# Kernel optimization log

Hardware: AMD Instinct MI355X
Metric: run time of the kernel (lower is better)

The kernel has to match this reference:

```python
import jax, jax.numpy as jnp
import numpy as np

F = 256

def setup_inputs() -> dict:
    key = jax.random.key(0)
    ks = jax.random.split(key, 6)
    s = 1.0 / np.sqrt(F)
    x = jax.random.normal(ks[0], (16, 1024, F), dtype=jnp.float32)
    W_alpha = jax.random.uniform(ks[1], (F, F), minval=-s, maxval=s, dtype=jnp.float32)
    W_beta = jax.random.uniform(ks[2], (F, F), minval=-s, maxval=s, dtype=jnp.float32)
    W_unary = jax.random.uniform(ks[3], (F, F), minval=-s, maxval=s, dtype=jnp.float32)
    b_unary = jax.random.uniform(ks[4], (F,), minval=-s, maxval=s, dtype=jnp.float32)
    W_r = jax.random.uniform(ks[5], (F, F), minval=-s, maxval=s, dtype=jnp.float32)
    return {"x": x, "W_alpha": W_alpha, "W_beta": W_beta, "W_unary": W_unary, "b_unary": b_unary, "W_r": W_r}

def reference(x, W_alpha, W_beta, W_unary, b_unary, W_r):
    # x: [B, N, F]; torch Linear computes x @ W^T (+ b)
    B, N, _ = x.shape
    alpha = jnp.einsum('bnf,gf->bng', x, W_alpha)
    beta = jnp.einsum('bnf,gf->bng', x, W_beta)
    unary = jnp.einsum('bnf,gf->bng', x, W_unary) + b_unary
    # scores: alpha_i . beta_j, diagonal excluded (i == j skipped in loop)
    scores = jnp.einsum('bif,bjf->bij', alpha, beta)
    scores = scores * (1.0 - jnp.eye(N, dtype=x.dtype))
    att = jnp.einsum('bij,bjf->bif', scores, unary) / N
    out = jnp.einsum('bif,gf->big', att, W_r) + x
    return out
```

## Files before the change

### kernel.cpp

```cpp
#include <hip/hip_runtime.h>


typedef __bf16 bf16;
typedef float floatx4 __attribute__((ext_vector_type(4)));
typedef bf16 bf16x8 __attribute__((ext_vector_type(8)));
typedef bf16 bf16x4 __attribute__((ext_vector_type(4)));

constexpr int FD = 256;
constexpr int NB = 16;
constexpr int NN = 1024;
constexpr int RR = NB * NN;

__device__ __forceinline__ bf16x8 cvt8(float4 a, float4 b) {
    bf16x8 o = { (bf16)a.x, (bf16)a.y, (bf16)a.z, (bf16)a.w,
                 (bf16)b.x, (bf16)b.y, (bf16)b.z, (bf16)b.w };
    return o;
}

__global__ __launch_bounds__(256)
void prep(const float* __restrict__ Wa, const float* __restrict__ Wb,
          const float* __restrict__ Wu, const float* __restrict__ bu,
          const float* __restrict__ Wr,
          bf16* __restrict__ Wcb, bf16* __restrict__ Wab, float* __restrict__ bc)
{
    const int blk = blockIdx.x, tid = threadIdx.x;
    if (blk < 256) {
        const int j = blk;
        float acc = 0.0f;
        for (int g = 0; g < FD; g += 4) {
            float4 wr = *(const float4*)&Wr[j * FD + g];
            acc += wr.x * Wu[g * FD + tid] + wr.y * Wu[(g + 1) * FD + tid]
                 + wr.z * Wu[(g + 2) * FD + tid] + wr.w * Wu[(g + 3) * FD + tid];
        }
        Wcb[j * FD + tid] = (bf16)acc;
    } else if (blk == 256) {
        float s = 0.0f;
        for (int g = 0; g < FD; g++) s += Wr[tid * FD + g] * bu[g];
        bc[tid] = s;
    } else {
        const int f = blk - 257;
        float acc = 0.0f;
        for (int k = 0; k < FD; k += 4) {
            acc += Wa[k * FD + f] * Wb[k * FD + tid]
                 + Wa[(k + 1) * FD + f] * Wb[(k + 1) * FD + tid]
                 + Wa[(k + 2) * FD + f] * Wb[(k + 2) * FD + tid]
                 + Wa[(k + 3) * FD + f] * Wb[(k + 3) * FD + tid];
        }
        Wab[f * FD + tid] = (bf16)acc;
    }
}

__global__ __launch_bounds__(256)
void proj2(const float* __restrict__ x,
           const bf16* __restrict__ Wab, const bf16* __restrict__ Wc,
           bf16* __restrict__ U2, bf16* __restrict__ abT, bf16* __restrict__ U2T,
           const float* __restrict__ bc, float* __restrict__ dpart)
{
    constexpr int BM = 128, BN = 64, BK = 32, LDK = 36;
    __shared__ bf16 As[BM][LDK];
    __shared__ bf16 Bs[2][BN][LDK];
    __shared__ bf16 Tr[8960];
    const int tid = threadIdx.x;
    const int wave = tid >> 6, lane = tid & 63;
    const int q = lane >> 4, l16 = lane & 15;
    const int bm = blockIdx.y * BM, bn = blockIdx.x * BN;

    const int rowA0 = tid >> 2,          k8A0 = (tid & 3) * 8;
    const int rowA1 = (tid + 256) >> 2,  k8A1 = (tid & 3) * 8;
    const int rowW  = tid >> 2,          k8W  = (tid & 3) * 8;

    bf16x8 pxa0, pxa1; int4 pwq, pwc;
#define PROJ_LOAD(KK) do { \
        const float* s0 = &x[(size_t)(bm + rowA0) * FD + (KK) + k8A0]; \
        pxa0 = cvt8(*(const float4*)s0, *(const float4*)(s0 + 4)); \
        const float* s1 = &x[(size_t)(bm + rowA1) * FD + (KK) + k8A1]; \
        pxa1 = cvt8(*(const float4*)s1, *(const float4*)(s1 + 4)); \
        pwq = *(const int4*)&Wab[(size_t)(bn + rowW) * FD + (KK) + k8W]; \
        pwc = *(const int4*)&Wc[(size_t)(bn + rowW) * FD + (KK) + k8W]; \
    } while (0)

    floatx4 acc[2][2][4] = {};
    PROJ_LOAD(0);

    for (int k0 = 0; k0 < FD; k0 += BK) {
        *(bf16x8*)&As[rowA0][k8A0] = pxa0;
        *(bf16x8*)&As[rowA1][k8A1] = pxa1;
        *(int4*)&Bs[0][rowW][k8W] = pwq;
        *(int4*)&Bs[1][rowW][k8W] = pwc;
        __syncthreads();
        if (k0 + BK < FD) PROJ_LOAD(k0 + BK);
        bf16x8 af[2];
        #pragma unroll
        for (int mi = 0; mi < 2; mi++)
            af[mi] = *(const bf16x8*)&As[wave * 32 + mi * 16 + l16][q * 8];
        #pragma unroll
        for (int w = 0; w < 2; w++) {
            bf16x8 bq[4];
            #pragma unroll
            for (int nj = 0; nj < 4; nj++)
                bq[nj] = *(const bf16x8*)&Bs[w][nj * 16 + l16][q * 8];
            #pragma unroll
            for (int mi = 0; mi < 2; mi++)
                #pragma unroll
                for (int nj = 0; nj < 4; nj++)
                    acc[w][mi][nj] = __builtin_amdgcn_mfma_f32_16x16x32_bf16(af[mi], bq[nj], acc[w][mi][nj], 0, 0, 0);
        }
        __syncthreads();
    }
#undef PROJ_LOAD

    const int b = bm >> 10, n0 = bm & (NN - 1);
    float bcv[4];
    #pragma unroll
    for (int nj = 0; nj < 4; nj++) bcv[nj] = bc[bn + nj * 16 + l16];

    #pragma unroll
    for (int mi = 0; mi < 2; mi++)
        #pragma unroll
        for (int i = 0; i < 4; i++) {
            const int m = bm + wave * 32 + mi * 16 + q * 4 + i;
            float p = 0.0f;
            #pragma unroll
            for (int nj = 0; nj < 4; nj++)
                p += x[(size_t)m * FD + bn + nj * 16 + l16] * acc[0][mi][nj][i];
            #pragma unroll
            for (int off = 1; off < 16; off <<= 1) p += __shfl_xor(p, off);
            if (l16 == 0) dpart[(size_t)blockIdx.x * RR + m] = p;
        }

    __syncthreads();
    #pragma unroll
    for (int mi = 0; mi < 2; mi++)
        #pragma unroll
        for (int i = 0; i < 4; i++) {
            int ml = wave * 32 + mi * 16 + q * 4 + i;
            #pragma unroll
            for (int nj = 0; nj < 4; nj++)
                Tr[ml * 68 + nj * 16 + l16] = (bf16)(acc[1][mi][nj][i] + bcv[nj]);
        }
    __syncthreads();
    #pragma unroll
    for (int it = 0; it < 4; it++) {
        int c = tid + it * 256;
        int row = c >> 3, chunk = c & 7;
        bf16x8 v = *(const bf16x8*)&Tr[row * 68 + chunk * 8];
        *(bf16x8*)&U2[(size_t)(bm + row) * FD + bn + chunk * 8] = v;
    }

    #pragma unroll
    for (int pass = 0; pass < 2; pass++) {
        __syncthreads();
        #pragma unroll
        for (int mi = 0; mi < 2; mi++)
            #pragma unroll
            for (int nj = 0; nj < 4; nj++) {
                bf16x4 v4;
                #pragma unroll
                for (int i = 0; i < 4; i++) {
                    float v = acc[pass][mi][nj][i];
                    if (pass == 1) v += bcv[nj];
                    v4[i] = (bf16)v;
                }
                *(bf16x4*)&Tr[(nj * 16 + l16) * 140 + wave * 32 + mi * 16 + q * 4] = v4;
            }
        __syncthreads();
        bf16* dst = (pass ? U2T : abT) + (size_t)b * FD * NN;
        #pragma unroll
        for (int it = 0; it < 4; it++) {
            int c = tid + it * 256;
            int row = c >> 4, chunk = c & 15;
            bf16x8 v = *(const bf16x8*)&Tr[row * 140 + chunk * 8];
            *(bf16x8*)&dst[(size_t)(bn + row) * NN + n0 + chunk * 8] = v;
        }
    }
}

__global__ __launch_bounds__(256)
void m2_mfma(const bf16* __restrict__ U2T, const bf16* __restrict__ abT, bf16* __restrict__ G)
{
    constexpr int LDK = 72;
    __shared__ bf16 As[64][LDK];
    __shared__ bf16 Bs[64][LDK];
    __shared__ bf16 Tr[64 * 68];
    const int tid = threadIdx.x;
    const int wave = tid >> 6, lane = tid & 63;
    const int q = lane >> 4, l16 = lane & 15;
    const int wj = wave >> 1, wk = wave & 1;
    const int b = blockIdx.z;
    const int bj = blockIdx.y * 64, bk = blockIdx.x * 64;
    const int r0 = tid >> 3,         k80 = (tid & 7) * 8;
    const int r1 = (tid + 256) >> 3, k81 = (tid & 7) * 8;
    const bf16* Arow0 = U2T + (size_t)b * FD * NN + (size_t)(bj + r0) * NN + k80;
    const bf16* Arow1 = U2T + (size_t)b * FD * NN + (size_t)(bj + r1) * NN + k81;
    const bf16* Brow0 = abT + (size_t)b * FD * NN + (size_t)(bk + r0) * NN + k80;
    const bf16* Brow1 = abT + (size_t)b * FD * NN + (size_t)(bk + r1) * NN + k81;

    int4 ra0 = *(const int4*)&Arow0[0];
    int4 ra1 = *(const int4*)&Arow1[0];
    int4 rb0 = *(const int4*)&Brow0[0];
    int4 rb1 = *(const int4*)&Brow1[0];
    floatx4 acc[2][2] = {};
    for (int n0 = 0; n0 < NN; n0 += 64) {
        *(int4*)&As[r0][k80] = ra0;
        *(int4*)&As[r1][k81] = ra1;
        *(int4*)&Bs[r0][k80] = rb0;
        *(int4*)&Bs[r1][k81] = rb1;
        __syncthreads();
        if (n0 + 64 < NN) {
            ra0 = *(const int4*)&Arow0[n0 + 64];
            ra1 = *(const int4*)&Arow1[n0 + 64];
            rb0 = *(const int4*)&Brow0[n0 + 64];
            rb1 = *(const int4*)&Brow1[n0 + 64];
        }
        #pragma unroll
        for (int kk = 0; kk < 2; kk++) {
            bf16x8 af[2], bq[2];
            #pragma unroll
            for (int mi = 0; mi < 2; mi++)
                af[mi] = *(const bf16x8*)&As[wj * 32 + mi * 16 + l16][kk * 32 + q * 8];
            #pragma unroll
            for (int kj = 0; kj < 2; kj++)
                bq[kj] = *(const bf16x8*)&Bs[wk * 32 + kj * 16 + l16][kk * 32 + q * 8];
            #pragma unroll
            for (int mi = 0; mi < 2; mi++)
                #pragma unroll
                for (int kj = 0; kj < 2; kj++)
                    acc[mi][kj] = __builtin_amdgcn_mfma_f32_16x16x32_bf16(af[mi], bq[kj], acc[mi][kj], 0, 0, 0);
        }
        __syncthreads();
    }
    __syncthreads();
    #pragma unroll
    for (int mi = 0; mi < 2; mi++)
        #pragma unroll
        for (int i = 0; i < 4; i++) {
            int jl = wj * 32 + mi * 16 + q * 4 + i;
            #pragma unroll
            for (int kj = 0; kj < 2; kj++)
                Tr[jl * 68 + wk * 32 + kj * 16 + l16] = (bf16)acc[mi][kj][i];
        }
    __syncthreads();
    bf16* Gb = G + (size_t)b * FD * FD;
    #pragma unroll
    for (int it = 0; it < 2; it++) {
        int c = tid + it * 256;
        int r = c >> 3, chunk = c & 7;
        bf16x8 v = *(const bf16x8*)&Tr[r * 68 + chunk * 8];
        *(bf16x8*)&Gb[(size_t)(bj + r) * FD + bk + chunk * 8] = v;
    }
}

__global__ __launch_bounds__(256)
void final_mfma(const float* __restrict__ x, const bf16* __restrict__ G,
                const float* __restrict__ dpart, const bf16* __restrict__ U2,
                float* __restrict__ out)
{
    constexpr int BM = 128, BN = 64, BK = 32, LDK = 36;
    __shared__ bf16 As[BM][LDK];
    __shared__ bf16 Bs[BN][LDK];
    const int tid = threadIdx.x;
    const int wave = tid >> 6, lane = tid & 63;
    const int q = lane >> 4, l16 = lane & 15;
    const int bm = blockIdx.y * BM, bn = blockIdx.x * BN;
    const bf16* Gb = G + (size_t)(bm >> 10) * FD * FD;

    const int rowA0 = tid >> 2,         k8A0 = (tid & 3) * 8;
    const int rowA1 = (tid + 256) >> 2, k8A1 = (tid & 3) * 8;
    const int rowB  = tid >> 2,         k8B  = (tid & 3) * 8;

    bf16x8 ra0, ra1; int4 rb;
#define FIN_LOAD(KK) do { \
        const float* s0 = &x[(size_t)(bm + rowA0) * FD + (KK) + k8A0]; \
        ra0 = cvt8(*(const float4*)s0, *(const float4*)(s0 + 4)); \
        const float* s1 = &x[(size_t)(bm + rowA1) * FD + (KK) + k8A1]; \
        ra1 = cvt8(*(const float4*)s1, *(const float4*)(s1 + 4)); \
        rb = *(const int4*)&Gb[(size_t)(bn + rowB) * FD + (KK) + k8B]; \
    } while (0)

    floatx4 acc[2][4] = {};
    FIN_LOAD(0);
    for (int k0 = 0; k0 < FD; k0 += BK) {
        *(bf16x8*)&As[rowA0][k8A0] = ra0;
        *(bf16x8*)&As[rowA1][k8A1] = ra1;
        *(int4*)&Bs[rowB][k8B] = rb;
        __syncthreads();
        if (k0 + BK < FD) FIN_LOAD(k0 + BK);
        bf16x8 af[2], bq[4];
        #pragma unroll
        for (int mi = 0; mi < 2; mi++)
            af[mi] = *(const bf16x8*)&As[wave * 32 + mi * 16 + l16][q * 8];
        #pragma unroll
        for (int nj = 0; nj < 4; nj++)
            bq[nj] = *(const bf16x8*)&Bs[nj * 16 + l16][q * 8];
        #pragma unroll
        for (int mi = 0; mi < 2; mi++)
            #pragma unroll
            for (int nj = 0; nj < 4; nj++)
                acc[mi][nj] = __builtin_amdgcn_mfma_f32_16x16x32_bf16(af[mi], bq[nj], acc[mi][nj], 0, 0, 0);
        __syncthreads();
    }
#undef FIN_LOAD

    #pragma unroll
    for (int mi = 0; mi < 2; mi++)
        #pragma unroll
        for (int i = 0; i < 4; i++) {
            int m = bm + wave * 32 + mi * 16 + q * 4 + i;
            float d = dpart[m] + dpart[RR + m] + dpart[2 * RR + m] + dpart[3 * RR + m];
            #pragma unroll
            for (int nj = 0; nj < 4; nj++) {
                int n = bn + nj * 16 + l16;
                float v = (acc[mi][nj][i] - d * (float)U2[(size_t)m * FD + n]) * (1.0f / 1024.0f);
                out[(size_t)m * FD + n] = v + x[(size_t)m * FD + n];
            }
        }
}

extern "C" void kernel_launch(void* const* d_in, const int* in_sizes, int n_in,
                              void* d_out, int out_size, void* d_ws, size_t ws_size,
                              hipStream_t stream)
{
    const float* x  = (const float*)d_in[0];
    const float* Wa = (const float*)d_in[1];
    const float* Wb = (const float*)d_in[2];
    const float* Wu = (const float*)d_in[3];
    const float* bu = (const float*)d_in[4];
    const float* Wr = (const float*)d_in[5];
    float* out = (float*)d_out;

    char* w = (char*)d_ws;
    bf16* Wcb   = (bf16*)w;  w += (size_t)FD * FD * 2;
    bf16* Wab   = (bf16*)w;  w += (size_t)FD * FD * 2;
    float* bc   = (float*)w; w += (size_t)FD * 4;
    bf16* U2    = (bf16*)w;  w += (size_t)RR * FD * 2;
    bf16* abT   = (bf16*)w;  w += (size_t)RR * FD * 2;
    bf16* U2T   = (bf16*)w;  w += (size_t)RR * FD * 2;
    bf16* G     = (bf16*)w;  w += (size_t)NB * FD * FD * 2;
    float* dpart= (float*)w; w += (size_t)4 * RR * 4;

    dim3 blk(256);

    prep<<<dim3(513), blk, 0, stream>>>(Wa, Wb, Wu, bu, Wr, Wcb, Wab, bc);

    proj2<<<dim3(FD / 64, RR / 128), blk, 0, stream>>>(x, Wab, Wcb,
                                                       U2, abT, U2T, bc, dpart);

    m2_mfma<<<dim3(FD / 64, FD / 64, NB), blk, 0, stream>>>(U2T, abT, G);

    final_mfma<<<dim3(FD / 64, RR / 128), blk, 0, stream>>>(x, G, dpart, U2, out);
}
```

Measured before the change: 133.0 us.

## Fuse projection, Gram and final kernels into one persistent kernel with grid barriers

Merges the three main kernels into a single 512-block kernel that uses atomic-counter grid barriers between phases, with shared memory overlaid through a union. The m2 stage is retiled to 64x32 output tiles so its work fills all 512 blocks. This removes two kernel launches and their tail gaps. In exchange the grid barrier spins on a global atomic, and the code relies on all 512 blocks being co-resident (launch bounds ask for two per CU), otherwise it can deadlock.

```diff
diff --git a/kernel.cpp b/kernel.cpp
--- a/kernel.cpp
+++ b/kernel.cpp
@@ -17,11 +17,28 @@
     return o;
 }
 
+struct P1s { bf16 As[128][36]; bf16 Bs[2][64][36]; bf16 Tr[8960]; };
+struct P2s { bf16 As[64][72];  bf16 Bs[32][72];    bf16 Tr[64*36]; };
+struct P3s { bf16 As[128][36]; bf16 Bs[64][36]; };
+union SMem { P1s p1; P2s p2; P3s p3; };
+
+__device__ __forceinline__ void grid_barrier(int* cnt, int target) {
+    __syncthreads();
+    if (threadIdx.x == 0) {
+        __threadfence();
+        __hip_atomic_fetch_add(cnt, 1, __ATOMIC_ACQ_REL, __HIP_MEMORY_SCOPE_AGENT);
+        while (__hip_atomic_load(cnt, __ATOMIC_ACQUIRE, __HIP_MEMORY_SCOPE_AGENT) < target)
+            __builtin_amdgcn_s_sleep(2);
+    }
+    __syncthreads();
+}
+
 __global__ __launch_bounds__(256)
 void prep(const float* __restrict__ Wa, const float* __restrict__ Wb,
           const float* __restrict__ Wu, const float* __restrict__ bu,
           const float* __restrict__ Wr,
-          bf16* __restrict__ Wcb, bf16* __restrict__ Wab, float* __restrict__ bc)
+          bf16* __restrict__ Wcb, bf16* __restrict__ Wab, float* __restrict__ bc,
+          int* __restrict__ cnt)
 {
     const int blk = blockIdx.x, tid = threadIdx.x;
     if (blk < 256) {
@@ -34,6 +51,7 @@
         }
         Wcb[j * FD + tid] = (bf16)acc;
     } else if (blk == 256) {
+        if (tid == 0) *cnt = 0;
         float s = 0.0f;
         for (int g = 0; g < FD; g++) s += Wr[tid * FD + g] * bu[g];
         bc[tid] = s;
@@ -50,20 +68,17 @@
     }
 }
 
-__global__ __launch_bounds__(256)
-void proj2(const float* __restrict__ x,
-           const bf16* __restrict__ Wab, const bf16* __restrict__ Wc,
-           bf16* __restrict__ U2, bf16* __restrict__ abT, bf16* __restrict__ U2T,
-           const float* __restrict__ bc, float* __restrict__ dpart)
-{
-    constexpr int BM = 128, BN = 64, BK = 32, LDK = 36;
-    __shared__ bf16 As[BM][LDK];
-    __shared__ bf16 Bs[2][BN][LDK];
-    __shared__ bf16 Tr[8960];
+__device__ void proj_tile(int bx, int by, P1s& s,
+                          const float* __restrict__ x,
+                          const bf16* __restrict__ Wab, const bf16* __restrict__ Wc,
+                          bf16* __restrict__ U2, bf16* __restrict__ abT, bf16* __restrict__ U2T,
+                          const float* __restrict__ bc, float* __restrict__ dpart)
+{
+    constexpr int BK = 32;
     const int tid = threadIdx.x;
     const int wave = tid >> 6, lane = tid & 63;
     const int q = lane >> 4, l16 = lane & 15;
-    const int bm = blockIdx.y * BM, bn = blockIdx.x * BN;
+    const int bm = by * 128, bn = bx * 64;
 
     const int rowA0 = tid >> 2,          k8A0 = (tid & 3) * 8;
     const int rowA1 = (tid + 256) >> 2,  k8A1 = (tid & 3) * 8;
@@ -83,22 +98,22 @@
     PROJ_LOAD(0);
 
     for (int k0 = 0; k0 < FD; k0 += BK) {
-        *(bf16x8*)&As[rowA0][k8A0] = pxa0;
-        *(bf16x8*)&As[rowA1][k8A1] = pxa1;
-        *(int4*)&Bs[0][rowW][k8W] = pwq;
-        *(int4*)&Bs[1][rowW][k8W] = pwc;
+        *(bf16x8*)&s.As[rowA0][k8A0] = pxa0;
+        *(bf16x8*)&s.As[rowA1][k8A1] = pxa1;
+        *(int4*)&s.Bs[0][rowW][k8W] = pwq;
+        *(int4*)&s.Bs[1][rowW][k8W] = pwc;
         __syncthreads();
         if (k0 + BK < FD) PROJ_LOAD(k0 + BK);
         bf16x8 af[2];
         #pragma unroll
         for (int mi = 0; mi < 2; mi++)
-            af[mi] = *(const bf16x8*)&As[wave * 32 + mi * 16 + l16][q * 8];
+            af[mi] = *(const bf16x8*)&s.As[wave * 32 + mi * 16 + l16][q * 8];
         #pragma unroll
         for (int w = 0; w < 2; w++) {
             bf16x8 bq[4];
             #pragma unroll
             for (int nj = 0; nj < 4; nj++)
-                bq[nj] = *(const bf16x8*)&Bs[w][nj * 16 + l16][q * 8];
+                bq[nj] = *(const bf16x8*)&s.Bs[w][nj * 16 + l16][q * 8];
             #pragma unroll
             for (int mi = 0; mi < 2; mi++)
                 #pragma unroll
@@ -125,7 +140,7 @@
                 p += x[(size_t)m * FD + bn + nj * 16 + l16] * acc[0][mi][nj][i];
             #pragma unroll
             for (int off = 1; off < 16; off <<= 1) p += __shfl_xor(p, off);
-            if (l16 == 0) dpart[(size_t)blockIdx.x * RR + m] = p;
+            if (l16 == 0) dpart[(size_t)bx * RR + m] = p;
         }
 
     __syncthreads();
@@ -136,14 +151,14 @@
             int ml = wave * 32 + mi * 16 + q * 4 + i;
             #pragma unroll
             for (int nj = 0; nj < 4; nj++)
-                Tr[ml * 68 + nj * 16 + l16] = (bf16)(acc[1][mi][nj][i] + bcv[nj]);
+                s.Tr[ml * 68 + nj * 16 + l16] = (bf16)(acc[1][mi][nj][i] + bcv[nj]);
         }
     __syncthreads();
     #pragma unroll
     for (int it = 0; it < 4; it++) {
         int c = tid + it * 256;
         int row = c >> 3, chunk = c & 7;
-        bf16x8 v = *(const bf16x8*)&Tr[row * 68 + chunk * 8];
+        bf16x8 v = *(const bf16x8*)&s.Tr[row * 68 + chunk * 8];
         *(bf16x8*)&U2[(size_t)(bm + row) * FD + bn + chunk * 8] = v;
     }
 
@@ -161,7 +176,7 @@
                     if (pass == 1) v += bcv[nj];
                     v4[i] = (bf16)v;
                 }
-                *(bf16x4*)&Tr[(nj * 16 + l16) * 140 + wave * 32 + mi * 16 + q * 4] = v4;
+                *(bf16x4*)&s.Tr[(nj * 16 + l16) * 140 + wave * 32 + mi * 16 + q * 4] = v4;
             }
         __syncthreads();
         bf16* dst = (pass ? U2T : abT) + (size_t)b * FD * NN;
@@ -169,99 +184,77 @@
         for (int it = 0; it < 4; it++) {
             int c = tid + it * 256;
             int row = c >> 4, chunk = c & 15;
-            bf16x8 v = *(const bf16x8*)&Tr[row * 140 + chunk * 8];
+            bf16x8 v = *(const bf16x8*)&s.Tr[row * 140 + chunk * 8];
             *(bf16x8*)&dst[(size_t)(bn + row) * NN + n0 + chunk * 8] = v;
         }
     }
 }
 
-__global__ __launch_bounds__(256)
-void m2_mfma(const bf16* __restrict__ U2T, const bf16* __restrict__ abT, bf16* __restrict__ G)
-{
-    constexpr int LDK = 72;
-    __shared__ bf16 As[64][LDK];
-    __shared__ bf16 Bs[64][LDK];
-    __shared__ bf16 Tr[64 * 68];
+__device__ void m2_tile(int bkt, int bjt, int b, P2s& s,
+                        const bf16* __restrict__ U2T, const bf16* __restrict__ abT,
+                        bf16* __restrict__ G)
+{
     const int tid = threadIdx.x;
     const int wave = tid >> 6, lane = tid & 63;
     const int q = lane >> 4, l16 = lane & 15;
-    const int wj = wave >> 1, wk = wave & 1;
-    const int b = blockIdx.z;
-    const int bj = blockIdx.y * 64, bk = blockIdx.x * 64;
-    const int r0 = tid >> 3,         k80 = (tid & 7) * 8;
-    const int r1 = (tid + 256) >> 3, k81 = (tid & 7) * 8;
-    const bf16* Arow0 = U2T + (size_t)b * FD * NN + (size_t)(bj + r0) * NN + k80;
-    const bf16* Arow1 = U2T + (size_t)b * FD * NN + (size_t)(bj + r1) * NN + k81;
-    const bf16* Brow0 = abT + (size_t)b * FD * NN + (size_t)(bk + r0) * NN + k80;
-    const bf16* Brow1 = abT + (size_t)b * FD * NN + (size_t)(bk + r1) * NN + k81;
+    const int bj = bjt * 64, bk = bkt * 32;
+    const int rA0 = tid >> 3, rA1 = rA0 + 32, k8 = (tid & 7) * 8;
+    const bf16* Arow0 = U2T + (size_t)b * FD * NN + (size_t)(bj + rA0) * NN + k8;
+    const bf16* Arow1 = U2T + (size_t)b * FD * NN + (size_t)(bj + rA1) * NN + k8;
+    const bf16* Brow  = abT + (size_t)b * FD * NN + (size_t)(bk + rA0) * NN + k8;
 
     int4 ra0 = *(const int4*)&Arow0[0];
     int4 ra1 = *(const int4*)&Arow1[0];
-    int4 rb0 = *(const int4*)&Brow0[0];
-    int4 rb1 = *(const int4*)&Brow1[0];
-    floatx4 acc[2][2] = {};
+    int4 rb  = *(const int4*)&Brow[0];
+    floatx4 acc[2] = {};
     for (int n0 = 0; n0 < NN; n0 += 64) {
-        *(int4*)&As[r0][k80] = ra0;
-        *(int4*)&As[r1][k81] = ra1;
-        *(int4*)&Bs[r0][k80] = rb0;
-        *(int4*)&Bs[r1][k81] = rb1;
+        *(int4*)&s.As[rA0][k8] = ra0;
+        *(int4*)&s.As[rA1][k8] = ra1;
+        *(int4*)&s.Bs[rA0][k8] = rb;
         __syncthreads();
         if (n0 + 64 < NN) {
             ra0 = *(const int4*)&Arow0[n0 + 64];
             ra1 = *(const int4*)&Arow1[n0 + 64];
-            rb0 = *(const int4*)&Brow0[n0 + 64];
-            rb1 = *(const int4*)&Brow1[n0 + 64];
+            rb  = *(const int4*)&Brow[n0 + 64];
         }
         #pragma unroll
         for (int kk = 0; kk < 2; kk++) {
-            bf16x8 af[2], bq[2];
-            #pragma unroll
-            for (int mi = 0; mi < 2; mi++)
-                af[mi] = *(const bf16x8*)&As[wj * 32 + mi * 16 + l16][kk * 32 + q * 8];
-            #pragma unroll
-            for (int kj = 0; kj < 2; kj++)
-                bq[kj] = *(const bf16x8*)&Bs[wk * 32 + kj * 16 + l16][kk * 32 + q * 8];
-            #pragma unroll
-            for (int mi = 0; mi < 2; mi++)
-                #pragma unroll
-                for (int kj = 0; kj < 2; kj++)
-                    acc[mi][kj] = __builtin_amdgcn_mfma_f32_16x16x32_bf16(af[mi], bq[kj], acc[mi][kj], 0, 0, 0);
-        }
-        __syncthreads();
-    }
-    __syncthreads();
-    #pragma unroll
-    for (int mi = 0; mi < 2; mi++)
-        #pragma unroll
-        for (int i = 0; i < 4; i++) {
-            int jl = wj * 32 + mi * 16 + q * 4 + i;
-            #pragma unroll
-            for (int kj = 0; kj < 2; kj++)
-                Tr[jl * 68 + wk * 32 + kj * 16 + l16] = (bf16)acc[mi][kj][i];
-        }
+            bf16x8 af = *(const bf16x8*)&s.As[wave * 16 + l16][kk * 32 + q * 8];
+            #pragma unroll
+            for (int kj = 0; kj < 2; kj++) {
+                bf16x8 bq = *(const bf16x8*)&s.Bs[kj * 16 + l16][kk * 32 + q * 8];
+                acc[kj] = __builtin_amdgcn_mfma_f32_16x16x32_bf16(af, bq, acc[kj], 0, 0, 0);
+            }
+        }
+        __syncthreads();
+    }
+    __syncthreads();
+    #pragma unroll
+    for (int i = 0; i < 4; i++) {
+        int jl = wave * 16 + q * 4 + i;
+        #pragma unroll
+        for (int kj = 0; kj < 2; kj++)
+            s.Tr[jl * 36 + kj * 16 + l16] = (bf16)acc[kj][i];
+    }
     __syncthreads();
     bf16* Gb = G + (size_t)b * FD * FD;
-    #pragma unroll
-    for (int it = 0; it < 2; it++) {
-        int c = tid + it * 256;
-        int r = c >> 3, chunk = c & 7;
-        bf16x8 v = *(const bf16x8*)&Tr[r * 68 + chunk * 8];
+    {
+        int r = tid >> 2, chunk = tid & 3;
+        bf16x8 v = *(const bf16x8*)&s.Tr[r * 36 + chunk * 8];
         *(bf16x8*)&Gb[(size_t)(bj + r) * FD + bk + chunk * 8] = v;
     }
 }
 
-__global__ __launch_bounds__(256)
-void final_mfma(const float* __restrict__ x, const bf16* __restrict__ G,
-                const float* __restrict__ dpart, const bf16* __restrict__ U2,
-                float* __restrict__ out)
-{
-    constexpr int BM = 128, BN = 64, BK = 32, LDK = 36;
-    __shared__ bf16 As[BM][LDK];
-    __shared__ bf16 Bs[BN][LDK];
+__device__ void final_tile(int bx, int by, P3s& s,
+                           const float* __restrict__ x, const bf16* __restrict__ G,
+                           const float* __restrict__ dpart, const bf16* __restrict__ U2,
+                           float* __restrict__ out)
+{
+    constexpr int BK = 32;
     const int tid = threadIdx.x;
     const int wave = tid >> 6, lane = tid & 63;
     const int q = lane >> 4, l16 = lane & 15;
-    const int bm = blockIdx.y * BM, bn = blockIdx.x * BN;
+    const int bm = by * 128, bn = bx * 64;
     const bf16* Gb = G + (size_t)(bm >> 10) * FD * FD;
 
     const int rowA0 = tid >> 2,         k8A0 = (tid & 3) * 8;
@@ -280,18 +273,18 @@
     floatx4 acc[2][4] = {};
     FIN_LOAD(0);
     for (int k0 = 0; k0 < FD; k0 += BK) {
-        *(bf16x8*)&As[rowA0][k8A0] = ra0;
-        *(bf16x8*)&As[rowA1][k8A1] = ra1;
-        *(int4*)&Bs[rowB][k8B] = rb;
+        *(bf16x8*)&s.As[rowA0][k8A0] = ra0;
+        *(bf16x8*)&s.As[rowA1][k8A1] = ra1;
+        *(int4*)&s.Bs[rowB][k8B] = rb;
         __syncthreads();
         if (k0 + BK < FD) FIN_LOAD(k0 + BK);
         bf16x8 af[2], bq[4];
         #pragma unroll
         for (int mi = 0; mi < 2; mi++)
-            af[mi] = *(const bf16x8*)&As[wave * 32 + mi * 16 + l16][q * 8];
+            af[mi] = *(const bf16x8*)&s.As[wave * 32 + mi * 16 + l16][q * 8];
         #pragma unroll
         for (int nj = 0; nj < 4; nj++)
-            bq[nj] = *(const bf16x8*)&Bs[nj * 16 + l16][q * 8];
+            bq[nj] = *(const bf16x8*)&s.Bs[nj * 16 + l16][q * 8];
         #pragma unroll
         for (int mi = 0; mi < 2; mi++)
             #pragma unroll
@@ -314,6 +307,28 @@
                 out[(size_t)m * FD + n] = v + x[(size_t)m * FD + n];
             }
         }
+}
+
+__global__ __launch_bounds__(256, 2)
+void mega(const float* __restrict__ x,
+          const bf16* __restrict__ Wab, const bf16* __restrict__ Wcb,
+          const float* __restrict__ bc,
+          bf16* __restrict__ U2, bf16* __restrict__ abT, bf16* __restrict__ U2T,
+          bf16* __restrict__ G, float* __restrict__ dpart,
+          float* __restrict__ out, int* __restrict__ cnt)
+{
+    __shared__ SMem sm;
+    const int bid = blockIdx.x;
+
+    proj_tile(bid & 3, bid >> 2, sm.p1, x, Wab, Wcb, U2, abT, U2T, bc, dpart);
+
+    grid_barrier(cnt, 512);
+
+    m2_tile(bid & 7, (bid >> 3) & 3, bid >> 5, sm.p2, U2T, abT, G);
+
+    grid_barrier(cnt, 1024);
+
+    final_tile(bid & 3, bid >> 2, sm.p3, x, G, dpart, U2, out);
 }
 
 extern "C" void kernel_launch(void* const* d_in, const int* in_sizes, int n_in,
@@ -337,15 +352,11 @@
     bf16* U2T   = (bf16*)w;  w += (size_t)RR * FD * 2;
     bf16* G     = (bf16*)w;  w += (size_t)NB * FD * FD * 2;
     float* dpart= (float*)w; w += (size_t)4 * RR * 4;
+    int* cnt    = (int*)w;   w += 256;
 
     dim3 blk(256);
 
-    prep<<<dim3(513), blk, 0, stream>>>(Wa, Wb, Wu, bu, Wr, Wcb, Wab, bc);
-
-    proj2<<<dim3(FD / 64, RR / 128), blk, 0, stream>>>(x, Wab, Wcb,
-                                                       U2, abT, U2T, bc, dpart);
-
-    m2_mfma<<<dim3(FD / 64, FD / 64, NB), blk, 0, stream>>>(U2T, abT, G);
-
-    final_mfma<<<dim3(FD / 64, RR / 128), blk, 0, stream>>>(x, G, dpart, U2, out);
-}
+    prep<<<dim3(513), blk, 0, stream>>>(Wa, Wb, Wu, bu, Wr, Wcb, Wab, bc, cnt);
+
+    mega<<<dim3(512), blk, 0, stream>>>(x, Wab, Wcb, bc, U2, abT, U2T, G, dpart, out, cnt);
+}
```

Result: slower. 259.7 us (+95.2%).

## Split-K the G gemm, double-buffer LDS, and shrink tiles for more blocks

Applied to the files above, without the earlier changes.

The m2 reduction over N is split into two halves written as fp32 partials, which doubles the grid from 256 to 512 blocks, and final_mfma sums the two partials while loading. proj and final_mfma drop from 128-row to 64-row tiles, doubling their block counts, and all three kernels get LDS double buffering with two-stage register prefetch and launch_bounds occupancy hints. The aim is to fill the GPU better and hide load latency. In exchange G traffic grows because it is stored in fp32 and twice, and the Wab/Wc weight tiles are reloaded by twice as many blocks.

```diff
diff --git a/kernel.cpp b/kernel.cpp
--- a/kernel.cpp
+++ b/kernel.cpp
@@ -10,6 +10,7 @@
 constexpr int NB = 16;
 constexpr int NN = 1024;
 constexpr int RR = NB * NN;
+constexpr int GH = NB * FD * FD;
 
 __device__ __forceinline__ bf16x8 cvt8(float4 a, float4 b) {
     bf16x8 o = { (bf16)a.x, (bf16)a.y, (bf16)a.z, (bf16)a.w,
@@ -50,64 +51,63 @@
     }
 }
 
-__global__ __launch_bounds__(256)
-void proj2(const float* __restrict__ x,
-           const bf16* __restrict__ Wab, const bf16* __restrict__ Wc,
-           bf16* __restrict__ U2, bf16* __restrict__ abT, bf16* __restrict__ U2T,
-           const float* __restrict__ bc, float* __restrict__ dpart)
-{
-    constexpr int BM = 128, BN = 64, BK = 32, LDK = 36;
-    __shared__ bf16 As[BM][LDK];
-    __shared__ bf16 Bs[2][BN][LDK];
-    __shared__ bf16 Tr[8960];
+__global__ __launch_bounds__(256, 4)
+void proj(const float* __restrict__ x,
+          const bf16* __restrict__ Wab, const bf16* __restrict__ Wc,
+          bf16* __restrict__ U2, bf16* __restrict__ abT, bf16* __restrict__ U2T,
+          const float* __restrict__ bc, float* __restrict__ dpart)
+{
+    __shared__ __align__(16) bf16 smem[13824];
+    typedef bf16 TileA[64][36];
+    typedef bf16 TileB[2][64][36];
+    TileA* As = (TileA*)smem;
+    TileB* Bs = (TileB*)(smem + 4608);
+    bf16*  Tr = smem;
+
     const int tid = threadIdx.x;
     const int wave = tid >> 6, lane = tid & 63;
     const int q = lane >> 4, l16 = lane & 15;
-    const int bm = blockIdx.y * BM, bn = blockIdx.x * BN;
-
-    const int rowA0 = tid >> 2,          k8A0 = (tid & 3) * 8;
-    const int rowA1 = (tid + 256) >> 2,  k8A1 = (tid & 3) * 8;
-    const int rowW  = tid >> 2,          k8W  = (tid & 3) * 8;
-
-    bf16x8 pxa0, pxa1; int4 pwq, pwc;
+    const int bm = blockIdx.y * 64, bn = blockIdx.x * 64;
+
+    const int row = tid >> 2, k8 = (tid & 3) * 8;
+
+    bf16x8 pxa; int4 pwq, pwc;
 #define PROJ_LOAD(KK) do { \
-        const float* s0 = &x[(size_t)(bm + rowA0) * FD + (KK) + k8A0]; \
-        pxa0 = cvt8(*(const float4*)s0, *(const float4*)(s0 + 4)); \
-        const float* s1 = &x[(size_t)(bm + rowA1) * FD + (KK) + k8A1]; \
-        pxa1 = cvt8(*(const float4*)s1, *(const float4*)(s1 + 4)); \
-        pwq = *(const int4*)&Wab[(size_t)(bn + rowW) * FD + (KK) + k8W]; \
-        pwc = *(const int4*)&Wc[(size_t)(bn + rowW) * FD + (KK) + k8W]; \
-    } while (0)
-
-    floatx4 acc[2][2][4] = {};
+        const float* s0 = &x[(size_t)(bm + row) * FD + (KK) + k8]; \
+        pxa = cvt8(*(const float4*)s0, *(const float4*)(s0 + 4)); \
+        pwq = *(const int4*)&Wab[(size_t)(bn + row) * FD + (KK) + k8]; \
+        pwc = *(const int4*)&Wc[(size_t)(bn + row) * FD + (KK) + k8]; \
+    } while (0)
+#define PROJ_STORE(BUF) do { \
+        *(bf16x8*)&As[BUF][row][k8] = pxa; \
+        *(int4*)&Bs[BUF][0][row][k8] = pwq; \
+        *(int4*)&Bs[BUF][1][row][k8] = pwc; \
+    } while (0)
+
+    floatx4 acc[2][4] = {};
     PROJ_LOAD(0);
-
-    for (int k0 = 0; k0 < FD; k0 += BK) {
-        *(bf16x8*)&As[rowA0][k8A0] = pxa0;
-        *(bf16x8*)&As[rowA1][k8A1] = pxa1;
-        *(int4*)&Bs[0][rowW][k8W] = pwq;
-        *(int4*)&Bs[1][rowW][k8W] = pwc;
-        __syncthreads();
-        if (k0 + BK < FD) PROJ_LOAD(k0 + BK);
-        bf16x8 af[2];
-        #pragma unroll
-        for (int mi = 0; mi < 2; mi++)
-            af[mi] = *(const bf16x8*)&As[wave * 32 + mi * 16 + l16][q * 8];
+    PROJ_STORE(0);
+    PROJ_LOAD(32);
+    __syncthreads();
+
+    #pragma unroll
+    for (int it = 0; it < 8; it++) {
+        const int cur = it & 1;
+        if (it + 1 < 8) PROJ_STORE(cur ^ 1);
+        if (it + 2 < 8) PROJ_LOAD((it + 2) * 32);
+        bf16x8 af = *(const bf16x8*)&As[cur][wave * 16 + l16][q * 8];
         #pragma unroll
         for (int w = 0; w < 2; w++) {
-            bf16x8 bq[4];
-            #pragma unroll
-            for (int nj = 0; nj < 4; nj++)
-                bq[nj] = *(const bf16x8*)&Bs[w][nj * 16 + l16][q * 8];
-            #pragma unroll
-            for (int mi = 0; mi < 2; mi++)
-                #pragma unroll
-                for (int nj = 0; nj < 4; nj++)
-                    acc[w][mi][nj] = __builtin_amdgcn_mfma_f32_16x16x32_bf16(af[mi], bq[nj], acc[w][mi][nj], 0, 0, 0);
+            #pragma unroll
+            for (int nj = 0; nj < 4; nj++) {
+                bf16x8 bq = *(const bf16x8*)&Bs[cur][w][nj * 16 + l16][q * 8];
+                acc[w][nj] = __builtin_amdgcn_mfma_f32_16x16x32_bf16(af, bq, acc[w][nj], 0, 0, 0);
+            }
         }
         __syncthreads();
     }
 #undef PROJ_LOAD
+#undef PROJ_STORE
 
     const int b = bm >> 10, n0 = bm & (NN - 1);
     float bcv[4];
@@ -115,112 +115,112 @@
     for (int nj = 0; nj < 4; nj++) bcv[nj] = bc[bn + nj * 16 + l16];
 
     #pragma unroll
-    for (int mi = 0; mi < 2; mi++)
-        #pragma unroll
-        for (int i = 0; i < 4; i++) {
-            const int m = bm + wave * 32 + mi * 16 + q * 4 + i;
-            float p = 0.0f;
-            #pragma unroll
-            for (int nj = 0; nj < 4; nj++)
-                p += x[(size_t)m * FD + bn + nj * 16 + l16] * acc[0][mi][nj][i];
-            #pragma unroll
-            for (int off = 1; off < 16; off <<= 1) p += __shfl_xor(p, off);
-            if (l16 == 0) dpart[(size_t)blockIdx.x * RR + m] = p;
-        }
-
+    for (int i = 0; i < 4; i++) {
+        const int m = bm + wave * 16 + q * 4 + i;
+        float p = 0.0f;
+        #pragma unroll
+        for (int nj = 0; nj < 4; nj++)
+            p += x[(size_t)m * FD + bn + nj * 16 + l16] * acc[0][nj][i];
+        #pragma unroll
+        for (int off = 1; off < 16; off <<= 1) p += __shfl_xor(p, off);
+        if (l16 == 0) dpart[(size_t)blockIdx.x * RR + m] = p;
+    }
+
+    #pragma unroll
+    for (int i = 0; i < 4; i++) {
+        int ml = wave * 16 + q * 4 + i;
+        #pragma unroll
+        for (int nj = 0; nj < 4; nj++)
+            Tr[ml * 72 + nj * 16 + l16] = (bf16)(acc[1][nj][i] + bcv[nj]);
+    }
     __syncthreads();
     #pragma unroll
-    for (int mi = 0; mi < 2; mi++)
-        #pragma unroll
-        for (int i = 0; i < 4; i++) {
-            int ml = wave * 32 + mi * 16 + q * 4 + i;
-            #pragma unroll
-            for (int nj = 0; nj < 4; nj++)
-                Tr[ml * 68 + nj * 16 + l16] = (bf16)(acc[1][mi][nj][i] + bcv[nj]);
-        }
-    __syncthreads();
-    #pragma unroll
-    for (int it = 0; it < 4; it++) {
+    for (int it = 0; it < 2; it++) {
         int c = tid + it * 256;
-        int row = c >> 3, chunk = c & 7;
-        bf16x8 v = *(const bf16x8*)&Tr[row * 68 + chunk * 8];
-        *(bf16x8*)&U2[(size_t)(bm + row) * FD + bn + chunk * 8] = v;
+        int r = c >> 3, chunk = c & 7;
+        bf16x8 v = *(const bf16x8*)&Tr[r * 72 + chunk * 8];
+        *(bf16x8*)&U2[(size_t)(bm + r) * FD + bn + chunk * 8] = v;
     }
 
     #pragma unroll
     for (int pass = 0; pass < 2; pass++) {
         __syncthreads();
         #pragma unroll
-        for (int mi = 0; mi < 2; mi++)
-            #pragma unroll
-            for (int nj = 0; nj < 4; nj++) {
-                bf16x4 v4;
-                #pragma unroll
-                for (int i = 0; i < 4; i++) {
-                    float v = acc[pass][mi][nj][i];
-                    if (pass == 1) v += bcv[nj];
-                    v4[i] = (bf16)v;
-                }
-                *(bf16x4*)&Tr[(nj * 16 + l16) * 140 + wave * 32 + mi * 16 + q * 4] = v4;
+        for (int nj = 0; nj < 4; nj++) {
+            bf16x4 v4;
+            #pragma unroll
+            for (int i = 0; i < 4; i++) {
+                float v = acc[pass][nj][i];
+                if (pass == 1) v += bcv[nj];
+                v4[i] = (bf16)v;
             }
+            *(bf16x4*)&Tr[(nj * 16 + l16) * 72 + wave * 16 + q * 4] = v4;
+        }
         __syncthreads();
         bf16* dst = (pass ? U2T : abT) + (size_t)b * FD * NN;
         #pragma unroll
-        for (int it = 0; it < 4; it++) {
+        for (int it = 0; it < 2; it++) {
             int c = tid + it * 256;
-            int row = c >> 4, chunk = c & 15;
-            bf16x8 v = *(const bf16x8*)&Tr[row * 140 + chunk * 8];
-            *(bf16x8*)&dst[(size_t)(bn + row) * NN + n0 + chunk * 8] = v;
-        }
-    }
-}
-
-__global__ __launch_bounds__(256)
-void m2_mfma(const bf16* __restrict__ U2T, const bf16* __restrict__ abT, bf16* __restrict__ G)
-{
-    constexpr int LDK = 72;
-    __shared__ bf16 As[64][LDK];
-    __shared__ bf16 Bs[64][LDK];
-    __shared__ bf16 Tr[64 * 68];
+            int r = c >> 3, chunk = c & 7;
+            bf16x8 v = *(const bf16x8*)&Tr[r * 72 + chunk * 8];
+            *(bf16x8*)&dst[(size_t)(bn + r) * NN + n0 + chunk * 8] = v;
+        }
+    }
+}
+
+__global__ __launch_bounds__(256, 4)
+void m2_mfma(const bf16* __restrict__ U2T, const bf16* __restrict__ abT, float* __restrict__ G)
+{
+    __shared__ __align__(16) bf16 smem[18432];
+    typedef bf16 TileM[64][72];
+    TileM* As = (TileM*)smem;
+    TileM* Bs = (TileM*)(smem + 9216);
+
     const int tid = threadIdx.x;
     const int wave = tid >> 6, lane = tid & 63;
     const int q = lane >> 4, l16 = lane & 15;
     const int wj = wave >> 1, wk = wave & 1;
-    const int b = blockIdx.z;
+    const int b = blockIdx.z >> 1, h = blockIdx.z & 1;
     const int bj = blockIdx.y * 64, bk = blockIdx.x * 64;
-    const int r0 = tid >> 3,         k80 = (tid & 7) * 8;
-    const int r1 = (tid + 256) >> 3, k81 = (tid & 7) * 8;
-    const bf16* Arow0 = U2T + (size_t)b * FD * NN + (size_t)(bj + r0) * NN + k80;
-    const bf16* Arow1 = U2T + (size_t)b * FD * NN + (size_t)(bj + r1) * NN + k81;
-    const bf16* Brow0 = abT + (size_t)b * FD * NN + (size_t)(bk + r0) * NN + k80;
-    const bf16* Brow1 = abT + (size_t)b * FD * NN + (size_t)(bk + r1) * NN + k81;
-
-    int4 ra0 = *(const int4*)&Arow0[0];
-    int4 ra1 = *(const int4*)&Arow1[0];
-    int4 rb0 = *(const int4*)&Brow0[0];
-    int4 rb1 = *(const int4*)&Brow1[0];
+    const int r0 = tid >> 3, r1 = r0 + 32, k8 = (tid & 7) * 8;
+
+    const bf16* Abase = U2T + (size_t)b * FD * NN + (size_t)h * 512;
+    const bf16* Bbase = abT + (size_t)b * FD * NN + (size_t)h * 512;
+    const bf16* Arow0 = Abase + (size_t)(bj + r0) * NN + k8;
+    const bf16* Arow1 = Abase + (size_t)(bj + r1) * NN + k8;
+    const bf16* Brow0 = Bbase + (size_t)(bk + r0) * NN + k8;
+    const bf16* Brow1 = Bbase + (size_t)(bk + r1) * NN + k8;
+
+    int4 ra0, ra1, rb0, rb1;
+#define M2_LOAD(NO) do { \
+        ra0 = *(const int4*)&Arow0[NO]; ra1 = *(const int4*)&Arow1[NO]; \
+        rb0 = *(const int4*)&Brow0[NO]; rb1 = *(const int4*)&Brow1[NO]; \
+    } while (0)
+#define M2_STORE(BUF) do { \
+        *(int4*)&As[BUF][r0][k8] = ra0; *(int4*)&As[BUF][r1][k8] = ra1; \
+        *(int4*)&Bs[BUF][r0][k8] = rb0; *(int4*)&Bs[BUF][r1][k8] = rb1; \
+    } while (0)
+
     floatx4 acc[2][2] = {};
-    for (int n0 = 0; n0 < NN; n0 += 64) {
-        *(int4*)&As[r0][k80] = ra0;
-        *(int4*)&As[r1][k81] = ra1;
-        *(int4*)&Bs[r0][k80] = rb0;
-        *(int4*)&Bs[r1][k81] = rb1;
-        __syncthreads();
-        if (n0 + 64 < NN) {
-            ra0 = *(const int4*)&Arow0[n0 + 64];
-            ra1 = *(const int4*)&Arow1[n0 + 64];
-            rb0 = *(const int4*)&Brow0[n0 + 64];
-            rb1 = *(const int4*)&Brow1[n0 + 64];
-        }
+    M2_LOAD(0);
+    M2_STORE(0);
+    M2_LOAD(64);
+    __syncthreads();
+
+    #pragma unroll
+    for (int it = 0; it < 8; it++) {
+        const int cur = it & 1;
+        if (it + 1 < 8) M2_STORE(cur ^ 1);
+        if (it + 2 < 8) M2_LOAD((it + 2) * 64);
         #pragma unroll
         for (int kk = 0; kk < 2; kk++) {
             bf16x8 af[2], bq[2];
             #pragma unroll
             for (int mi = 0; mi < 2; mi++)
-                af[mi] = *(const bf16x8*)&As[wj * 32 + mi * 16 + l16][kk * 32 + q * 8];
+                af[mi] = *(const bf16x8*)&As[cur][wj * 32 + mi * 16 + l16][kk * 32 + q * 8];
             #pragma unroll
             for (int kj = 0; kj < 2; kj++)
-                bq[kj] = *(const bf16x8*)&Bs[wk * 32 + kj * 16 + l16][kk * 32 + q * 8];
+                bq[kj] = *(const bf16x8*)&Bs[cur][wk * 32 + kj * 16 + l16][kk * 32 + q * 8];
             #pragma unroll
             for (int mi = 0; mi < 2; mi++)
                 #pragma unroll
@@ -229,91 +229,90 @@
         }
         __syncthreads();
     }
-    __syncthreads();
+#undef M2_LOAD
+#undef M2_STORE
+
+    float* Gb = G + (size_t)h * GH + (size_t)b * FD * FD;
     #pragma unroll
     for (int mi = 0; mi < 2; mi++)
         #pragma unroll
         for (int i = 0; i < 4; i++) {
-            int jl = wj * 32 + mi * 16 + q * 4 + i;
-            #pragma unroll
-            for (int kj = 0; kj < 2; kj++)
-                Tr[jl * 68 + wk * 32 + kj * 16 + l16] = (bf16)acc[mi][kj][i];
-        }
-    __syncthreads();
-    bf16* Gb = G + (size_t)b * FD * FD;
-    #pragma unroll
-    for (int it = 0; it < 2; it++) {
-        int c = tid + it * 256;
-        int r = c >> 3, chunk = c & 7;
-        bf16x8 v = *(const bf16x8*)&Tr[r * 68 + chunk * 8];
-        *(bf16x8*)&Gb[(size_t)(bj + r) * FD + bk + chunk * 8] = v;
-    }
-}
-
-__global__ __launch_bounds__(256)
-void final_mfma(const float* __restrict__ x, const bf16* __restrict__ G,
+            int j = wj * 32 + mi * 16 + q * 4 + i;
+            #pragma unroll
+            for (int kj = 0; kj < 2; kj++) {
+                int k = wk * 32 + kj * 16 + l16;
+                Gb[(size_t)(bj + j) * FD + bk + k] = acc[mi][kj][i];
+            }
+        }
+}
+
+__global__ __launch_bounds__(256, 4)
+void final_mfma(const float* __restrict__ x, const float* __restrict__ G,
                 const float* __restrict__ dpart, const bf16* __restrict__ U2,
                 float* __restrict__ out)
 {
-    constexpr int BM = 128, BN = 64, BK = 32, LDK = 36;
-    __shared__ bf16 As[BM][LDK];
-    __shared__ bf16 Bs[BN][LDK];
+    __shared__ __align__(16) bf16 smem[9216];
+    typedef bf16 TileA[64][36];
+    TileA* As = (TileA*)smem;
+    TileA* Bs = (TileA*)(smem + 4608);
+
     const int tid = threadIdx.x;
     const int wave = tid >> 6, lane = tid & 63;
     const int q = lane >> 4, l16 = lane & 15;
-    const int bm = blockIdx.y * BM, bn = blockIdx.x * BN;
-    const bf16* Gb = G + (size_t)(bm >> 10) * FD * FD;
-
-    const int rowA0 = tid >> 2,         k8A0 = (tid & 3) * 8;
-    const int rowA1 = (tid + 256) >> 2, k8A1 = (tid & 3) * 8;
-    const int rowB  = tid >> 2,         k8B  = (tid & 3) * 8;
-
-    bf16x8 ra0, ra1; int4 rb;
+    const int bm = blockIdx.y * 64, bn = blockIdx.x * 64;
+    const float* Gb = G + (size_t)(bm >> 10) * FD * FD;
+
+    const int row = tid >> 2, k8 = (tid & 3) * 8;
+
+    bf16x8 ra, rb;
 #define FIN_LOAD(KK) do { \
-        const float* s0 = &x[(size_t)(bm + rowA0) * FD + (KK) + k8A0]; \
-        ra0 = cvt8(*(const float4*)s0, *(const float4*)(s0 + 4)); \
-        const float* s1 = &x[(size_t)(bm + rowA1) * FD + (KK) + k8A1]; \
-        ra1 = cvt8(*(const float4*)s1, *(const float4*)(s1 + 4)); \
-        rb = *(const int4*)&Gb[(size_t)(bn + rowB) * FD + (KK) + k8B]; \
-    } while (0)
-
-    floatx4 acc[2][4] = {};
+        const float* s0 = &x[(size_t)(bm + row) * FD + (KK) + k8]; \
+        ra = cvt8(*(const float4*)s0, *(const float4*)(s0 + 4)); \
+        const float* g0 = &Gb[(size_t)(bn + row) * FD + (KK) + k8]; \
+        float4 p0 = *(const float4*)g0, p1 = *(const float4*)(g0 + 4); \
+        float4 q0 = *(const float4*)(g0 + GH), q1 = *(const float4*)(g0 + GH + 4); \
+        float4 u = { p0.x + q0.x, p0.y + q0.y, p0.z + q0.z, p0.w + q0.w }; \
+        float4 v = { p1.x + q1.x, p1.y + q1.y, p1.z + q1.z, p1.w + q1.w }; \
+        rb = cvt8(u, v); \
+    } while (0)
+#define FIN_STORE(BUF) do { \
+        *(bf16x8*)&As[BUF][row][k8] = ra; \
+        *(bf16x8*)&Bs[BUF][row][k8] = rb; \
+    } while (0)
+
+    floatx4 acc[4] = {};
     FIN_LOAD(0);
-    for (int k0 = 0; k0 < FD; k0 += BK) {
-        *(bf16x8*)&As[rowA0][k8A0] = ra0;
-        *(bf16x8*)&As[rowA1][k8A1] = ra1;
-        *(int4*)&Bs[rowB][k8B] = rb;
-        __syncthreads();
-        if (k0 + BK < FD) FIN_LOAD(k0 + BK);
-        bf16x8 af[2], bq[4];
-        #pragma unroll
-        for (int mi = 0; mi < 2; mi++)
-            af[mi] = *(const bf16x8*)&As[wave * 32 + mi * 16 + l16][q * 8];
-        #pragma unroll
-        for (int nj = 0; nj < 4; nj++)
-            bq[nj] = *(const bf16x8*)&Bs[nj * 16 + l16][q * 8];
-        #pragma unroll
-        for (int mi = 0; mi < 2; mi++)
-            #pragma unroll
-            for (int nj = 0; nj < 4; nj++)
-                acc[mi][nj] = __builtin_amdgcn_mfma_f32_16x16x32_bf16(af[mi], bq[nj], acc[mi][nj], 0, 0, 0);
+    FIN_STORE(0);
+    FIN_LOAD(32);
+    __syncthreads();
+
+    #pragma unroll
+    for (int it = 0; it < 8; it++) {
+        const int cur = it & 1;
+        if (it + 1 < 8) FIN_STORE(cur ^ 1);
+        if (it + 2 < 8) FIN_LOAD((it + 2) * 32);
+        bf16x8 af = *(const bf16x8*)&As[cur][wave * 16 + l16][q * 8];
+        #pragma unroll
+        for (int nj = 0; nj < 4; nj++) {
+            bf16x8 bq = *(const bf16x8*)&Bs[cur][nj * 16 + l16][q * 8];
+            acc[nj] = __builtin_amdgcn_mfma_f32_16x16x32_bf16(af, bq, acc[nj], 0, 0, 0);
+        }
         __syncthreads();
     }
 #undef FIN_LOAD
-
-    #pragma unroll
-    for (int mi = 0; mi < 2; mi++)
-        #pragma unroll
-        for (int i = 0; i < 4; i++) {
-            int m = bm + wave * 32 + mi * 16 + q * 4 + i;
-            float d = dpart[m] + dpart[RR + m] + dpart[2 * RR + m] + dpart[3 * RR + m];
-            #pragma unroll
-            for (int nj = 0; nj < 4; nj++) {
-                int n = bn + nj * 16 + l16;
-                float v = (acc[mi][nj][i] - d * (float)U2[(size_t)m * FD + n]) * (1.0f / 1024.0f);
-                out[(size_t)m * FD + n] = v + x[(size_t)m * FD + n];
-            }
-        }
+#undef FIN_STORE
+
+    #pragma unroll
+    for (int i = 0; i < 4; i++) {
+        int m = bm + wave * 16 + q * 4 + i;
+        float d = dpart[m] + dpart[RR + m] + dpart[2 * RR + m] + dpart[3 * RR + m];
+        #pragma unroll
+        for (int nj = 0; nj < 4; nj++) {
+            int n = bn + nj * 16 + l16;
+            float v = (acc[nj][i] - d * (float)U2[(size_t)m * FD + n]) * (1.0f / 1024.0f);
+            out[(size_t)m * FD + n] = v + x[(size_t)m * FD + n];
+        }
+    }
 }
 
 extern "C" void kernel_launch(void* const* d_in, const int* in_sizes, int n_in,
@@ -335,17 +334,16 @@
     bf16* U2    = (bf16*)w;  w += (size_t)RR * FD * 2;
     bf16* abT   = (bf16*)w;  w += (size_t)RR * FD * 2;
     bf16* U2T   = (bf16*)w;  w += (size_t)RR * FD * 2;
-    bf16* G     = (bf16*)w;  w += (size_t)NB * FD * FD * 2;
+    float* G    = (float*)w; w += (size_t)2 * GH * 4;
     float* dpart= (float*)w; w += (size_t)4 * RR * 4;
 
     dim3 blk(256);
 
     prep<<<dim3(513), blk, 0, stream>>>(Wa, Wb, Wu, bu, Wr, Wcb, Wab, bc);
 
-    proj2<<<dim3(FD / 64, RR / 128), blk, 0, stream>>>(x, Wab, Wcb,
-                                                       U2, abT, U2T, bc, dpart);
-
-    m2_mfma<<<dim3(FD / 64, FD / 64, NB), blk, 0, stream>>>(U2T, abT, G);
-
-    final_mfma<<<dim3(FD / 64, RR / 128), blk, 0, stream>>>(x, G, dpart, U2, out);
-}
+    proj<<<dim3(4, 256), blk, 0, stream>>>(x, Wab, Wcb, U2, abT, U2T, bc, dpart);
+
+    m2_mfma<<<dim3(4, 4, 32), blk, 0, stream>>>(U2T, abT, G);
+
+    final_mfma<<<dim3(4, 256), blk, 0, stream>>>(x, G, dpart, U2, out);
+}
```

Result: slower. 176.6 us (+32.8%).
